# Kernel tuning notes

Hardware: AMD Instinct MI355X
Metric: run time of the kernel (lower is better)

## Reference

```python
import jax, jax.numpy as jnp
import numpy as np

BINS = 5
POINTS = 2
EPS_DIV = 1e-6
GN_GROUPS = 32
GN_EPS = 1e-5


def bilinear_sum(img, ys, xs):
    """Sum of bilinear samples with zero padding outside the image.
    img: (B, C, H, W); ys, xs: (B, K, H, W) absolute sample coords.
    Returns (B, C, H, W) = sum over K of bilinear(img, ys_k, xs_k)."""
    B, C, H, W = img.shape
    K = ys.shape[1]
    y0 = jnp.floor(ys)
    x0 = jnp.floor(xs)
    imgf = img.reshape(B, C, H * W)
    acc = jnp.zeros((B, C, K, H, W), img.dtype)
    for dy, dx in ((0, 0), (0, 1), (1, 0), (1, 1)):
        yi = y0 + dy
        xi = x0 + dx
        w = (1.0 - jnp.abs(ys - yi)) * (1.0 - jnp.abs(xs - xi))
        valid = (yi >= 0) & (yi <= H - 1) & (xi >= 0) & (xi <= W - 1)
        yc = jnp.clip(yi, 0, H - 1).astype(jnp.int32)
        xc = jnp.clip(xi, 0, W - 1).astype(jnp.int32)
        idx = (yc * W + xc).reshape(B, 1, K * H * W)
        g = jnp.take_along_axis(imgf, idx, axis=2).reshape(B, C, K, H, W)
        acc = acc + (w * valid.astype(img.dtype))[:, None] * g
    return acc.sum(axis=2)


def setup_inputs():
    key = jax.random.key(0)
    ks = jax.random.split(key, 6)
    B, C, H, W = 2, 256, 100, 152
    P, K = POINTS, BINS
    x = jax.random.normal(ks[0], (B, C, H, W), jnp.float32)
    offsets = jax.random.normal(ks[1], (B, P * K * 2, H, W), jnp.float32) * 2.0
    ef_w = jax.random.normal(ks[2], (P * C, C), jnp.float32) * 0.02
    ef_b = jnp.zeros((P * C,), jnp.float32)
    hm1_w = jax.random.normal(ks[3], (P, C, C), jnp.float32) * 0.02
    hm1_b = jnp.zeros((P, C), jnp.float32)
    hm2_w = jax.random.normal(ks[4], (P, C), jnp.float32) * 0.02
    hm2_b = jnp.zeros((P,), jnp.float32)
    merge_w = jax.random.normal(ks[5], (C, P * C), jnp.float32) * 0.02
    merge_b = jnp.zeros((C,), jnp.float32)
    gn_g = jnp.ones((C,), jnp.float32)
    gn_b = jnp.zeros((C,), jnp.float32)
    return {"x": x, "offsets": offsets, "ef_w": ef_w, "ef_b": ef_b,
            "hm1_w": hm1_w, "hm1_b": hm1_b, "hm2_w": hm2_w, "hm2_b": hm2_b,
            "merge_w": merge_w, "merge_b": merge_b, "gn_g": gn_g, "gn_b": gn_b}


def reference(x, offsets, ef_w, ef_b, hm1_w, hm1_b, hm2_w, hm2_b, merge_w, merge_b, gn_g, gn_b):
    B, C, H, W = x.shape
    P, K = POINTS, BINS
    # expand_feat: 1x1 conv C -> P*C
    ef = jnp.einsum('bchw,dc->bdhw', x, ef_w) + ef_b[None, :, None, None]
    efp = ef.reshape(B, P, C, H, W)
    # heatmap: grouped 1x1 conv (per-point) -> ReLU -> grouped 1x1 conv -> exp
    h = jax.nn.relu(jnp.einsum('bpchw,pdc->bpdhw', efp, hm1_w) + hm1_b[None, :, :, None, None])
    heat = jnp.exp(jnp.einsum('bpdhw,pd->bphw', h, hm2_w) + hm2_b[None, :, None, None])  # (B,P,H,W)
    # offsets: (B, P, K, 2, H, W) with channel layout [y, x] per bin.
    # base_offset cancels the [1,bins] kernel grid, so the deform conv with
    # all-ones weights is simply: sum over bins of bilinear samples at
    # (h + off_y, w + off_x).
    off = offsets.reshape(B, P, K, 2, H, W)
    hg = jnp.arange(H, dtype=x.dtype)[None, None, None, :, None]
    wg = jnp.arange(W, dtype=x.dtype)[None, None, None, None, :]
    ys = hg + off[:, :, :, 0]  # (B,P,K,H,W)
    xs = wg + off[:, :, :, 1]
    outs = []
    for p in range(P):
        # sample feat*heat (C channels) and heat (1 channel) together
        img = jnp.concatenate([efp[:, p] * heat[:, p][:, None], heat[:, p][:, None]], axis=1)
        s = bilinear_sum(img, ys[:, p], xs[:, p])  # (B, C+1, H, W)
        outs.append(s[:, :C] / (s[:, C:] + EPS_DIV))
    outs = jnp.concatenate(outs, axis=1)  # (B, P*C, H, W)
    merged = jnp.einsum('bchw,dc->bdhw', outs, merge_w) + merge_b[None, :, None, None]
    # GroupNorm(32, C) + ReLU
    g = merged.reshape(B, GN_GROUPS, C // GN_GROUPS, H, W)
    mu = g.mean(axis=(2, 3, 4), keepdims=True)
    var = g.var(axis=(2, 3, 4), keepdims=True)
    gn = ((g - mu) / jnp.sqrt(var + GN_EPS)).reshape(B, C, H, W)
    gn = gn * gn_g[None, :, None, None] + gn_b[None, :, None, None]
    return jax.nn.relu(gn)
```

## Files before the change

kernel.cpp:

```cpp
#include <hip/hip_runtime.h>

#define BINS 5
#define PTS  2
constexpr int Bx = 2, Cc = 256, Hh = 100, Ww = 152;
constexpr int HW = Hh * Ww;
constexpr int NTILE = 238;
constexpr float EPS_DIV = 1e-6f;
constexpr float GN_EPS  = 1e-5f;

typedef __attribute__((ext_vector_type(8)))  _Float16 hfrag;
typedef __attribute__((ext_vector_type(2)))  _Float16 h2;
typedef __attribute__((ext_vector_type(16))) float    f32x16;

__device__ __forceinline__ ushort f2h(float f) {
    return __builtin_bit_cast(ushort, (_Float16)f);
}
__device__ __forceinline__ float hlo(unsigned u) {
    return (float)__builtin_bit_cast(_Float16, (ushort)(u & 0xffffu));
}
__device__ __forceinline__ float hhi(unsigned u) {
    return (float)__builtin_bit_cast(_Float16, (ushort)(u >> 16));
}

#define GLL16(g, l) __builtin_amdgcn_global_load_lds( \
    (const __attribute__((address_space(1))) unsigned*)(g), \
    (__attribute__((address_space(3))) unsigned*)(l), 16, 0, 0)

#define MFMA32(a, b, c) __builtin_amdgcn_mfma_f32_32x32x16_f16(a, b, c, 0, 0, 0)

__global__ __launch_bounds__(256)
void k_wconv(const float* __restrict__ efw, const float* __restrict__ w1,
             const float* __restrict__ mw, ushort* __restrict__ wb)
{
    int gid = blockIdx.x * 256 + threadIdx.x;
    int i = gid * 8;
    int arr = i >> 17, off = i & 131071;
    const float* src = arr == 0 ? efw : (arr == 1 ? w1 : mw);
    float4 v0 = *(const float4*)(src + off);
    float4 v1 = *(const float4*)(src + off + 4);
    int outaddr;
    if (arr == 0) {
        int m = off >> 8, k = off & 255;
        outaddr = (((k >> 4) * 16 + (m >> 5)) * 64 + (m & 31) + 32 * ((k >> 3) & 1)) * 8;
    } else if (arr == 1) {
        int p = off >> 16, r = off & 65535;
        int m = r >> 8, k = r & 255;
        outaddr = p * 65536 +
                  (((k >> 4) * 8 + (m >> 5)) * 64 + (m & 31) + 32 * ((k >> 3) & 1)) * 8;
    } else {
        int m = off >> 9, k = off & 511;
        outaddr = (((k >> 4) * 8 + (m >> 5)) * 64 + (m & 31) + 32 * ((k >> 3) & 1)) * 8;
    }
    ushort o[8] = { f2h(v0.x), f2h(v0.y), f2h(v0.z), f2h(v0.w),
                    f2h(v1.x), f2h(v1.y), f2h(v1.z), f2h(v1.w) };
    *(uint4*)(wb + arr * 131072 + outaddr) = *(uint4*)o;
}

__global__ __launch_bounds__(256)
void k_xt(const float* __restrict__ x, ushort* __restrict__ xbt)
{
    __shared__ float tile[32][33];
    const int t = threadIdx.x;
    const int hw0 = blockIdx.x * 32;
    const int c0 = blockIdx.y * 32;
    const int b = blockIdx.z;
    const float* xb = x + ((size_t)b * Cc + c0) * HW + hw0;
    const int tx = t & 31, ty = t >> 5;
    #pragma unroll
    for (int r = 0; r < 4; r++) {
        int c = ty + r * 8;
        tile[c][tx] = xb[(size_t)c * HW + tx];
    }
    __syncthreads();
    const int hwl = t >> 3, c4 = (t & 7) * 4;
    ushort4 o = { f2h(tile[c4 + 0][hwl]), f2h(tile[c4 + 1][hwl]),
                  f2h(tile[c4 + 2][hwl]), f2h(tile[c4 + 3][hwl]) };
    *(ushort4*)&xbt[((size_t)b * HW + hw0 + hwl) * Cc + c0 + c4] = o;
}

__global__ __launch_bounds__(512, 2)
void k_ef(const ushort* __restrict__ xbt, const ushort* __restrict__ wbe,
          const float* __restrict__ efb, ushort* __restrict__ efp)
{
    __shared__ ushort B0[64 * 256];
    __shared__ ushort B1[64 * 256];
    const int t = threadIdx.x;
    const int wv = t >> 6, ln = t & 63;
    const int l31 = ln & 31, lh = ln >> 5;
    const int b = blockIdx.y;
    const int tt0 = blockIdx.x * 2;
    const ushort* xb = xbt + (size_t)b * HW * Cc;

    hfrag A[2][16];
    #pragma unroll
    for (int mf = 0; mf < 2; mf++)
        #pragma unroll
        for (int ks = 0; ks < 16; ks++)
            A[mf][ks] = *(const hfrag*)&wbe[((ks * 16 + (wv * 2 + mf)) * 64 + ln) * 8];
    __builtin_amdgcn_sched_barrier(0);

    auto stageB = [&](int tt, ushort* dst) {
        int tp0 = tt * 64;
        #pragma unroll
        for (int j = 0; j < 4; j++) {
            int unit = j * 512 + t;
            int prow = unit >> 5, c8 = unit & 31;
            int pq = tp0 + prow; if (pq > HW - 1) pq = HW - 1;
            const ushort* g = xb + (size_t)pq * Cc + ((c8 ^ (prow & 7)) << 3);
            ushort* l = dst + (j * 512 + wv * 64) * 8;
            GLL16(g, l);
        }
    };
    stageB(tt0, B0);
    stageB(tt0 + 1, B1);
    __builtin_amdgcn_sched_barrier(0);
    asm volatile("s_waitcnt vmcnt(4)" ::: "memory");
    __builtin_amdgcn_s_barrier();
    __builtin_amdgcn_sched_barrier(0);

    auto compute = [&](int tt, const ushort* Bs) {
        f32x16 acc[2][2];
        #pragma unroll
        for (int mf = 0; mf < 2; mf++)
            #pragma unroll
            for (int pf = 0; pf < 2; pf++)
                #pragma unroll
                for (int r = 0; r < 16; r++) acc[mf][pf][r] = 0.f;
        #pragma unroll
        for (int ks = 0; ks < 16; ks++) {
            int c = ks * 2 + lh;
            #pragma unroll
            for (int pf = 0; pf < 2; pf++) {
                hfrag bf = *(const hfrag*)&Bs[(pf * 32 + l31) * 256 + ((c ^ (l31 & 7)) << 3)];
                acc[0][pf] = MFMA32(A[0][ks], bf, acc[0][pf]);
                acc[1][pf] = MFMA32(A[1][ks], bf, acc[1][pf]);
            }
        }
        const int tp0 = tt * 64;
        const int p_ = wv >> 2;
        ushort* outb = efp + (size_t)((b * PTS + p_) * HW) * Cc;
        #pragma unroll
        for (int mf = 0; mf < 2; mf++) {
            int m0 = wv * 2 + mf;
            int chb = (m0 * 32) & 255;
            #pragma unroll
            for (int q = 0; q < 4; q++) {
                float4 bv = *(const float4*)&efb[m0 * 32 + q * 8 + 4 * lh];
                #pragma unroll
                for (int pf = 0; pf < 2; pf++) {
                    int px = tp0 + pf * 32 + l31;
                    if (px < HW) {
                        int ch = chb + q * 8 + 4 * lh;
                        ushort4 o = { f2h(acc[mf][pf][q * 4 + 0] + bv.x),
                                      f2h(acc[mf][pf][q * 4 + 1] + bv.y),
                                      f2h(acc[mf][pf][q * 4 + 2] + bv.z),
                                      f2h(acc[mf][pf][q * 4 + 3] + bv.w) };
                        *(ushort4*)&outb[(size_t)px * Cc + ch] = o;
                    }
                }
            }
        }
    };
    compute(tt0, B0);
    asm volatile("s_waitcnt vmcnt(0)" ::: "memory");
    __builtin_amdgcn_s_barrier();
    __builtin_amdgcn_sched_barrier(0);
    compute(tt0 + 1, B1);
}

__global__ __launch_bounds__(512, 2)
void k_heat(const ushort* __restrict__ efp, const ushort* __restrict__ wb1,
            const float* __restrict__ b1, const float* __restrict__ w2,
            const float* __restrict__ b2, float* __restrict__ heat)
{
    __shared__ ushort B0[64 * 256];
    __shared__ ushort B1[64 * 256];
    __shared__ float red[8][64];
    const int t = threadIdx.x;
    const int wv = t >> 6, ln = t & 63;
    const int l31 = ln & 31, lh = ln >> 5;
    const int zz = blockIdx.y;
    const int b = zz >> 1, p = zz & 1;
    const int tt0 = blockIdx.x * 2;
    const ushort* eb = efp + (size_t)((b * PTS + p) * HW) * Cc;
    const float* b1p = b1 + p * 256;
    const float* w2p = w2 + p * 256;
    const float b2v = b2[p];

    hfrag A[16];
    #pragma unroll
    for (int ks = 0; ks < 16; ks++)
        A[ks] = *(const hfrag*)&wb1[p * 65536 + ((ks * 8 + wv) * 64 + ln) * 8];
    __builtin_amdgcn_sched_barrier(0);

    auto stageB = [&](int tt, ushort* dst) {
        int tp0 = tt * 64;
        #pragma unroll
        for (int j = 0; j < 4; j++) {
            int unit = j * 512 + t;
            int prow = unit >> 5, c8 = unit & 31;
            int pq = tp0 + prow; if (pq > HW - 1) pq = HW - 1;
            const ushort* g = eb + (size_t)pq * Cc + ((c8 ^ (prow & 7)) << 3);
            ushort* l = dst + (j * 512 + wv * 64) * 8;
            GLL16(g, l);
        }
    };
    stageB(tt0, B0);
    stageB(tt0 + 1, B1);
    __builtin_amdgcn_sched_barrier(0);
    asm volatile("s_waitcnt vmcnt(4)" ::: "memory");
    __builtin_amdgcn_s_barrier();
    __builtin_amdgcn_sched_barrier(0);

    auto compute = [&](int tt, const ushort* Bs) {
        f32x16 acc[2];
        #pragma unroll
        for (int pf = 0; pf < 2; pf++)
            #pragma unroll
            for (int r = 0; r < 16; r++) acc[pf][r] = 0.f;
        #pragma unroll
        for (int ks = 0; ks < 16; ks++) {
            int c = ks * 2 + lh;
            #pragma unroll
            for (int pf = 0; pf < 2; pf++) {
                hfrag bf = *(const hfrag*)&Bs[(pf * 32 + l31) * 256 + ((c ^ (l31 & 7)) << 3)];
                acc[pf] = MFMA32(A[ks], bf, acc[pf]);
            }
        }
        float s[2] = {0.f, 0.f};
        #pragma unroll
        for (int q = 0; q < 4; q++) {
            float4 b1v = *(const float4*)&b1p[wv * 32 + q * 8 + 4 * lh];
            float4 w2v = *(const float4*)&w2p[wv * 32 + q * 8 + 4 * lh];
            #pragma unroll
            for (int pf = 0; pf < 2; pf++) {
                float h0 = acc[pf][q * 4 + 0] + b1v.x;
                float h1 = acc[pf][q * 4 + 1] + b1v.y;
                float h2_ = acc[pf][q * 4 + 2] + b1v.z;
                float h3 = acc[pf][q * 4 + 3] + b1v.w;
                s[pf] += w2v.x * (h0 > 0.f ? h0 : 0.f);
                s[pf] += w2v.y * (h1 > 0.f ? h1 : 0.f);
                s[pf] += w2v.z * (h2_ > 0.f ? h2_ : 0.f);
                s[pf] += w2v.w * (h3 > 0.f ? h3 : 0.f);
            }
        }
        s[0] += __shfl_xor(s[0], 32);
        s[1] += __shfl_xor(s[1], 32);
        if (lh == 0) {
            red[wv][l31]      = s[0];
            red[wv][32 + l31] = s[1];
        }
        asm volatile("s_waitcnt lgkmcnt(0)" ::: "memory");
        __builtin_amdgcn_s_barrier();
        if (t < 64) {
            float v = red[0][t] + red[1][t] + red[2][t] + red[3][t] +
                      red[4][t] + red[5][t] + red[6][t] + red[7][t];
            int px = tt * 64 + t;
            if (px < HW) heat[(size_t)(b * PTS + p) * HW + px] = expf(v + b2v);
        }
    };
    compute(tt0, B0);
    asm volatile("s_waitcnt vmcnt(0)" ::: "memory");
    __builtin_amdgcn_s_barrier();
    __builtin_amdgcn_sched_barrier(0);
    compute(tt0 + 1, B1);
}

__global__ __launch_bounds__(256)
void k_sample(const ushort* __restrict__ efp, const float* __restrict__ heat,
              const float* __restrict__ offs, ushort* __restrict__ outs)
{
    __shared__ uint2 s_wo[32][20];
    const int t = threadIdx.x;
    const int bid = blockIdx.x;
    const int nx = (bid & 7) * 60 + (bid >> 3);
    if (nx >= 475) return;
    const int m0 = nx * 32;
    const int p = blockIdx.y;
    const int b = blockIdx.z;
    const float* heat_bp = heat + (size_t)(b * PTS + p) * HW;

    if (t < 32 * BINS) {
        int j = t / BINS, k = t % BINS;
        int hw = m0 + j;
        int hh = hw / Ww, ww = hw % Ww;
        int chy = (p * BINS + k) * 2;
        float oy = offs[((size_t)b * (PTS * BINS * 2) + chy)     * HW + hw];
        float ox = offs[((size_t)b * (PTS * BINS * 2) + chy + 1) * HW + hw];
        float ysf = (float)hh + oy;
        float xsf = (float)ww + ox;
        float y0 = floorf(ysf), x0 = floorf(xsf);
        #pragma unroll
        for (int dy = 0; dy < 2; dy++)
            #pragma unroll
            for (int dx = 0; dx < 2; dx++) {
                float yi = y0 + dy, xi = x0 + dx;
                float wgt = (1.f - fabsf(ysf - yi)) * (1.f - fabsf(xsf - xi));
                bool valid = (yi >= 0.f) && (yi <= (float)(Hh - 1)) &&
                             (xi >= 0.f) && (xi <= (float)(Ww - 1));
                int yc = (int)yi; yc = yc < 0 ? 0 : (yc > Hh - 1 ? Hh - 1 : yc);
                int xc = (int)xi; xc = xc < 0 ? 0 : (xc > Ww - 1 ? Ww - 1 : xc);
                int idx = yc * Ww + xc;
                float wh = valid ? wgt * heat_bp[idx] : 0.f;
                s_wo[j][k * 4 + dy * 2 + dx] =
                    make_uint2(__float_as_uint(wh), (unsigned)idx << 9);
            }
    }
    __syncthreads();
    if (t < 32) {
        float s = 0.f;
        #pragma unroll
        for (int u = 0; u < 20; u++) s += __uint_as_float(s_wo[t][u].x);
        float inv = 1.f / (s + EPS_DIV);
        #pragma unroll
        for (int u = 0; u < 20; u++) {
            float w = __uint_as_float(s_wo[t][u].x) * inv;
            unsigned hw16 = (unsigned)f2h(w);
            s_wo[t][u].x = hw16 | (hw16 << 16);
        }
    }
    __syncthreads();

    const int wv = t >> 6, ln = t & 63;
    const int half = ln >> 5, c8 = ln & 31;
    const char* efbase = (const char*)(efp + (size_t)((b * PTS + p) * HW) * Cc)
                         + c8 * 16;
    ushort* ob = outs + ((size_t)(b * HW + m0)) * (PTS * Cc) + p * Cc + c8 * 8;
    #pragma unroll
    for (int i = 0; i < 8; i += 2) {
        const int j = wv * 8 + i + half;
        h2 a0 = (h2){0, 0}, a1 = (h2){0, 0}, a2 = (h2){0, 0}, a3 = (h2){0, 0};
        #pragma unroll
        for (int u = 0; u < 20; u++) {
            uint2 wo = s_wo[j][u];
            uint4 v = *(const uint4*)(efbase + wo.y);
            h2 wp = __builtin_bit_cast(h2, wo.x);
            a0 += wp * __builtin_bit_cast(h2, v.x);
            a1 += wp * __builtin_bit_cast(h2, v.y);
            a2 += wp * __builtin_bit_cast(h2, v.z);
            a3 += wp * __builtin_bit_cast(h2, v.w);
        }
        uint4 o = { __builtin_bit_cast(unsigned, a0), __builtin_bit_cast(unsigned, a1),
                    __builtin_bit_cast(unsigned, a2), __builtin_bit_cast(unsigned, a3) };
        *(uint4*)(ob + (size_t)j * (PTS * Cc)) = o;
    }
}

__global__ __launch_bounds__(512, 2)
void k_merge(const ushort* __restrict__ outs, const ushort* __restrict__ wbm,
             const float* __restrict__ mb, ushort* __restrict__ mgb,
             float* __restrict__ part2)
{
    __shared__ ushort B0[64 * 512];
    __shared__ ushort B1[64 * 512];
    const int t = threadIdx.x;
    const int wv = t >> 6, ln = t & 63;
    const int l31 = ln & 31, lh = ln >> 5;
    const int b = blockIdx.y;
    const int tt0 = blockIdx.x * 2;
    const ushort* ob = outs + (size_t)b * HW * (PTS * Cc);

    hfrag A[32];
    #pragma unroll
    for (int ks = 0; ks < 32; ks++)
        A[ks] = *(const hfrag*)&wbm[((ks * 8 + wv) * 64 + ln) * 8];
    __builtin_amdgcn_sched_barrier(0);

    auto stageB = [&](int tt, ushort* dst) {
        int tp0 = tt * 64;
        #pragma unroll
        for (int j = 0; j < 8; j++) {
            int unit = j * 512 + t;
            int prow = unit >> 6, c8 = unit & 63;
            int pq = tp0 + prow; if (pq > HW - 1) pq = HW - 1;
            const ushort* g = ob + (size_t)pq * (PTS * Cc) + ((c8 ^ (prow & 7)) << 3);
            ushort* l = dst + (j * 512 + wv * 64) * 8;
            GLL16(g, l);
        }
    };
    stageB(tt0, B0);
    stageB(tt0 + 1, B1);
    __builtin_amdgcn_sched_barrier(0);
    asm volatile("s_waitcnt vmcnt(8)" ::: "memory");
    __builtin_amdgcn_s_barrier();
    __builtin_amdgcn_sched_barrier(0);

    auto compute = [&](int tt, const ushort* Bs) {
        f32x16 acc[2];
        #pragma unroll
        for (int pf = 0; pf < 2; pf++)
            #pragma unroll
            for (int r = 0; r < 16; r++) acc[pf][r] = 0.f;
        #pragma unroll
        for (int ks = 0; ks < 32; ks++) {
            int c = ks * 2 + lh;
            #pragma unroll
            for (int pf = 0; pf < 2; pf++) {
                hfrag bf = *(const hfrag*)&Bs[(pf * 32 + l31) * 512 + ((c ^ (l31 & 7)) << 3)];
                acc[pf] = MFMA32(A[ks], bf, acc[pf]);
            }
        }
        const int tp0 = tt * 64;
        float sg[4] = {0.f, 0.f, 0.f, 0.f};
        float qg[4] = {0.f, 0.f, 0.f, 0.f};
        #pragma unroll
        for (int q = 0; q < 4; q++) {
            float4 bv = *(const float4*)&mb[wv * 32 + q * 8 + 4 * lh];
            #pragma unroll
            for (int pf = 0; pf < 2; pf++) {
                int px = tp0 + pf * 32 + l31;
                if (px < HW) {
                    #pragma unroll
                    for (int r = 0; r < 4; r++) {
                        float bb = r == 0 ? bv.x : (r == 1 ? bv.y : (r == 2 ? bv.z : bv.w));
                        float v = acc[pf][q * 4 + r] + bb;
                        int ch = wv * 32 + q * 8 + 4 * lh + r;
                        mgb[((size_t)b * Cc + ch) * HW + px] = f2h(v);
                        sg[q] += v; qg[q] += v * v;
                    }
                }
            }
        }
        #pragma unroll
        for (int q = 0; q < 4; q++) {
            #pragma unroll
            for (int off = 1; off <= 32; off <<= 1) {
                sg[q] += __shfl_xor(sg[q], off);
                qg[q] += __shfl_xor(qg[q], off);
            }
        }
        if (ln == 0) {
            #pragma unroll
            for (int q = 0; q < 4; q++) {
                int g = wv * 4 + q;
                size_t idx = ((size_t)(b * 32 + g) * NTILE + tt) * 2;
                part2[idx + 0] = sg[q];
                part2[idx + 1] = qg[q];
            }
        }
    };
    compute(tt0, B0);
    asm volatile("s_waitcnt vmcnt(0)" ::: "memory");
    __builtin_amdgcn_s_barrier();
    __builtin_amdgcn_sched_barrier(0);
    compute(tt0 + 1, B1);
}

__global__ __launch_bounds__(256)
void k_gnfinal(const float* __restrict__ part2, float* __restrict__ statf)
{
    const int bg = blockIdx.x;
    const int t = threadIdx.x;
    float s = 0.f, q = 0.f;
    if (t < NTILE) {
        s = part2[((size_t)bg * NTILE + t) * 2 + 0];
        q = part2[((size_t)bg * NTILE + t) * 2 + 1];
    }
    #pragma unroll
    for (int off = 1; off <= 32; off <<= 1) {
        s += __shfl_xor(s, off);
        q += __shfl_xor(q, off);
    }
    __shared__ float rs[4], rq[4];
    int wid = t >> 6;
    if ((t & 63) == 0) { rs[wid] = s; rq[wid] = q; }
    __syncthreads();
    if (t == 0) {
        float S = rs[0] + rs[1] + rs[2] + rs[3];
        float Q = rq[0] + rq[1] + rq[2] + rq[3];
        const float n = 8.f * HW;
        float mean = S / n;
        float var  = Q / n - mean * mean;
        statf[bg * 2 + 0] = mean;
        statf[bg * 2 + 1] = rsqrtf(var + GN_EPS);
    }
}

__global__ __launch_bounds__(256)
void k_gnapply(const ushort* __restrict__ mgb, const float* __restrict__ statf,
               const float* __restrict__ gg, const float* __restrict__ gb,
               float* __restrict__ out)
{
    const int i8 = blockIdx.x * 256 + threadIdx.x;
    const int i = i8 * 8;
    const int CHW = Cc * HW;
    const int b = i / CHW;
    const int r = i - b * CHW;
    const int c = r / HW;
    const int g = c >> 3;
    float mean = statf[(b * 32 + g) * 2 + 0];
    float istd = statf[(b * 32 + g) * 2 + 1];
    float sc = istd * gg[c];
    float sh = gb[c] - mean * sc;
    uint4 v = *(const uint4*)(mgb + i);
    float4 o0, o1;
    o0.x = fmaxf(hlo(v.x) * sc + sh, 0.f);
    o0.y = fmaxf(hhi(v.x) * sc + sh, 0.f);
    o0.z = fmaxf(hlo(v.y) * sc + sh, 0.f);
    o0.w = fmaxf(hhi(v.y) * sc + sh, 0.f);
    o1.x = fmaxf(hlo(v.z) * sc + sh, 0.f);
    o1.y = fmaxf(hhi(v.z) * sc + sh, 0.f);
    o1.z = fmaxf(hlo(v.w) * sc + sh, 0.f);
    o1.w = fmaxf(hhi(v.w) * sc + sh, 0.f);
    *(float4*)(out + i)     = o0;
    *(float4*)(out + i + 4) = o1;
}

extern "C" void kernel_launch(void* const* d_in, const int* in_sizes, int n_in,
                              void* d_out, int out_size, void* d_ws, size_t ws_size,
                              hipStream_t stream)
{
    const float* x    = (const float*)d_in[0];
    const float* offs = (const float*)d_in[1];
    const float* efw  = (const float*)d_in[2];
    const float* efb  = (const float*)d_in[3];
    const float* w1   = (const float*)d_in[4];
    const float* b1   = (const float*)d_in[5];
    const float* w2   = (const float*)d_in[6];
    const float* b2   = (const float*)d_in[7];
    const float* mw   = (const float*)d_in[8];
    const float* mb   = (const float*)d_in[9];
    const float* gg   = (const float*)d_in[10];
    const float* gb   = (const float*)d_in[11];
    float* out = (float*)d_out;

    ushort* wb    = (ushort*)d_ws;
    ushort* wbe   = wb;
    ushort* wb1   = wb + 131072;
    ushort* wbm   = wb + 262144;
    ushort* efp   = wb + 393216;
    ushort* outsb = efp + (size_t)Bx * PTS * HW * Cc;
    ushort* xbt   = outsb + (size_t)Bx * HW * PTS * Cc;
    ushort* mgb   = xbt + (size_t)Bx * HW * Cc;
    float*  heat  = (float*)(mgb + (size_t)Bx * Cc * HW);
    float*  part2 = heat + (size_t)Bx * PTS * HW;
    float*  statf = part2 + (size_t)64 * NTILE * 2;

    dim3 blk(256);
    k_wconv  <<<dim3(192),              blk, 0, stream>>>(efw, w1, mw, wb);
    k_xt     <<<dim3(475, 8, Bx),       blk, 0, stream>>>(x, xbt);
    k_ef     <<<dim3(119, Bx),    dim3(512), 0, stream>>>(xbt, wbe, efb, efp);
    k_heat   <<<dim3(119, 4),     dim3(512), 0, stream>>>(efp, wb1, b1, w2, b2, heat);
    k_sample <<<dim3(480, PTS, Bx),     blk, 0, stream>>>(efp, heat, offs, outsb);
    k_merge  <<<dim3(119, Bx),    dim3(512), 0, stream>>>(outsb, wbm, mb, mgb, part2);
    k_gnfinal<<<dim3(64),               blk, 0, stream>>>(part2, statf);
    k_gnapply<<<dim3(Bx * Cc * HW / 8 / 256), blk, 0, stream>>>(mgb, statf, gg, gb, out);
}
```

Baseline: 206.3 us.

## Fuse bilinear sampling into merge GEMM and merge weight/input prep kernels

The sampling stage now writes its per-tile results straight into a swizzled LDS buffer, and the merge MFMA GEMM reads its B operand from there, so the intermediate sampled-feature tensor no longer round-trips through global memory. Merge weights are loaded in chunks of eight fragments to cut register pressure. The weight conversion and input transpose kernels are combined into one launch. The fused kernel loses the previous double-buffered async global-to-LDS prefetch and serialises sampling, barriers and GEMM inside each block, which may leave fewer blocks in flight. The ef output-point index is also now derived per fragment (m0>>3) rather than per wave.

```diff
diff --git a/kernel.cpp b/kernel.cpp
--- a/kernel.cpp
+++ b/kernel.cpp
@@ -29,53 +29,54 @@
 #define MFMA32(a, b, c) __builtin_amdgcn_mfma_f32_32x32x16_f16(a, b, c, 0, 0, 0)
 
 __global__ __launch_bounds__(256)
-void k_wconv(const float* __restrict__ efw, const float* __restrict__ w1,
-             const float* __restrict__ mw, ushort* __restrict__ wb)
-{
-    int gid = blockIdx.x * 256 + threadIdx.x;
-    int i = gid * 8;
-    int arr = i >> 17, off = i & 131071;
-    const float* src = arr == 0 ? efw : (arr == 1 ? w1 : mw);
-    float4 v0 = *(const float4*)(src + off);
-    float4 v1 = *(const float4*)(src + off + 4);
-    int outaddr;
-    if (arr == 0) {
-        int m = off >> 8, k = off & 255;
-        outaddr = (((k >> 4) * 16 + (m >> 5)) * 64 + (m & 31) + 32 * ((k >> 3) & 1)) * 8;
-    } else if (arr == 1) {
-        int p = off >> 16, r = off & 65535;
-        int m = r >> 8, k = r & 255;
-        outaddr = p * 65536 +
-                  (((k >> 4) * 8 + (m >> 5)) * 64 + (m & 31) + 32 * ((k >> 3) & 1)) * 8;
+void k_pre(const float* __restrict__ efw, const float* __restrict__ w1,
+           const float* __restrict__ mw, ushort* __restrict__ wb,
+           const float* __restrict__ x, ushort* __restrict__ xbt)
+{
+    __shared__ float tile[32][33];
+    const int bid = blockIdx.x;
+    const int t = threadIdx.x;
+    if (bid < 192) {
+        int gid = bid * 256 + t;
+        int i = gid * 8;
+        int arr = i >> 17, off = i & 131071;
+        const float* src = arr == 0 ? efw : (arr == 1 ? w1 : mw);
+        float4 v0 = *(const float4*)(src + off);
+        float4 v1 = *(const float4*)(src + off + 4);
+        int outaddr;
+        if (arr == 0) {
+            int m = off >> 8, k = off & 255;
+            outaddr = (((k >> 4) * 16 + (m >> 5)) * 64 + (m & 31) + 32 * ((k >> 3) & 1)) * 8;
+        } else if (arr == 1) {
+            int p = off >> 16, r = off & 65535;
+            int m = r >> 8, k = r & 255;
+            outaddr = p * 65536 +
+                      (((k >> 4) * 8 + (m >> 5)) * 64 + (m & 31) + 32 * ((k >> 3) & 1)) * 8;
+        } else {
+            int m = off >> 9, k = off & 511;
+            outaddr = (((k >> 4) * 8 + (m >> 5)) * 64 + (m & 31) + 32 * ((k >> 3) & 1)) * 8;
+        }
+        ushort o[8] = { f2h(v0.x), f2h(v0.y), f2h(v0.z), f2h(v0.w),
+                        f2h(v1.x), f2h(v1.y), f2h(v1.z), f2h(v1.w) };
+        *(uint4*)(wb + arr * 131072 + outaddr) = *(uint4*)o;
     } else {
-        int m = off >> 9, k = off & 511;
-        outaddr = (((k >> 4) * 8 + (m >> 5)) * 64 + (m & 31) + 32 * ((k >> 3) & 1)) * 8;
-    }
-    ushort o[8] = { f2h(v0.x), f2h(v0.y), f2h(v0.z), f2h(v0.w),
-                    f2h(v1.x), f2h(v1.y), f2h(v1.z), f2h(v1.w) };
-    *(uint4*)(wb + arr * 131072 + outaddr) = *(uint4*)o;
-}
-
-__global__ __launch_bounds__(256)
-void k_xt(const float* __restrict__ x, ushort* __restrict__ xbt)
-{
-    __shared__ float tile[32][33];
-    const int t = threadIdx.x;
-    const int hw0 = blockIdx.x * 32;
-    const int c0 = blockIdx.y * 32;
-    const int b = blockIdx.z;
-    const float* xb = x + ((size_t)b * Cc + c0) * HW + hw0;
-    const int tx = t & 31, ty = t >> 5;
-    #pragma unroll
-    for (int r = 0; r < 4; r++) {
-        int c = ty + r * 8;
-        tile[c][tx] = xb[(size_t)c * HW + tx];
-    }
-    __syncthreads();
-    const int hwl = t >> 3, c4 = (t & 7) * 4;
-    ushort4 o = { f2h(tile[c4 + 0][hwl]), f2h(tile[c4 + 1][hwl]),
-                  f2h(tile[c4 + 2][hwl]), f2h(tile[c4 + 3][hwl]) };
-    *(ushort4*)&xbt[((size_t)b * HW + hw0 + hwl) * Cc + c0 + c4] = o;
+        int r = bid - 192;
+        const int b = r / 3800; r -= b * 3800;
+        const int c0 = (r / 475) * 32;
+        const int hw0 = (r % 475) * 32;
+        const float* xb = x + ((size_t)b * Cc + c0) * HW + hw0;
+        const int tx = t & 31, ty = t >> 5;
+        #pragma unroll
+        for (int rr = 0; rr < 4; rr++) {
+            int c = ty + rr * 8;
+            tile[c][tx] = xb[(size_t)c * HW + tx];
+        }
+        __syncthreads();
+        const int hwl = t >> 3, c4 = (t & 7) * 4;
+        ushort4 o = { f2h(tile[c4 + 0][hwl]), f2h(tile[c4 + 1][hwl]),
+                      f2h(tile[c4 + 2][hwl]), f2h(tile[c4 + 3][hwl]) };
+        *(ushort4*)&xbt[((size_t)b * HW + hw0 + hwl) * Cc + c0 + c4] = o;
+    }
 }
 
 __global__ __launch_bounds__(512, 2)
@@ -137,11 +138,11 @@
             }
         }
         const int tp0 = tt * 64;
-        const int p_ = wv >> 2;
-        ushort* outb = efp + (size_t)((b * PTS + p_) * HW) * Cc;
         #pragma unroll
         for (int mf = 0; mf < 2; mf++) {
             int m0 = wv * 2 + mf;
+            const int p_ = m0 >> 3;
+            ushort* outb = efp + (size_t)((b * PTS + p_) * HW) * Cc;
             int chb = (m0 * 32) & 255;
             #pragma unroll
             for (int q = 0; q < 4; q++) {
@@ -266,184 +267,158 @@
     compute(tt0 + 1, B1);
 }
 
-__global__ __launch_bounds__(256)
-void k_sample(const ushort* __restrict__ efp, const float* __restrict__ heat,
-              const float* __restrict__ offs, ushort* __restrict__ outs)
-{
-    __shared__ uint2 s_wo[32][20];
-    const int t = threadIdx.x;
-    const int bid = blockIdx.x;
-    const int nx = (bid & 7) * 60 + (bid >> 3);
-    if (nx >= 475) return;
-    const int m0 = nx * 32;
-    const int p = blockIdx.y;
-    const int b = blockIdx.z;
-    const float* heat_bp = heat + (size_t)(b * PTS + p) * HW;
-
-    if (t < 32 * BINS) {
-        int j = t / BINS, k = t % BINS;
-        int hw = m0 + j;
-        int hh = hw / Ww, ww = hw % Ww;
-        int chy = (p * BINS + k) * 2;
-        float oy = offs[((size_t)b * (PTS * BINS * 2) + chy)     * HW + hw];
-        float ox = offs[((size_t)b * (PTS * BINS * 2) + chy + 1) * HW + hw];
-        float ysf = (float)hh + oy;
-        float xsf = (float)ww + ox;
-        float y0 = floorf(ysf), x0 = floorf(xsf);
-        #pragma unroll
-        for (int dy = 0; dy < 2; dy++)
-            #pragma unroll
-            for (int dx = 0; dx < 2; dx++) {
-                float yi = y0 + dy, xi = x0 + dx;
-                float wgt = (1.f - fabsf(ysf - yi)) * (1.f - fabsf(xsf - xi));
-                bool valid = (yi >= 0.f) && (yi <= (float)(Hh - 1)) &&
-                             (xi >= 0.f) && (xi <= (float)(Ww - 1));
-                int yc = (int)yi; yc = yc < 0 ? 0 : (yc > Hh - 1 ? Hh - 1 : yc);
-                int xc = (int)xi; xc = xc < 0 ? 0 : (xc > Ww - 1 ? Ww - 1 : xc);
-                int idx = yc * Ww + xc;
-                float wh = valid ? wgt * heat_bp[idx] : 0.f;
-                s_wo[j][k * 4 + dy * 2 + dx] =
-                    make_uint2(__float_as_uint(wh), (unsigned)idx << 9);
-            }
-    }
-    __syncthreads();
-    if (t < 32) {
-        float s = 0.f;
-        #pragma unroll
-        for (int u = 0; u < 20; u++) s += __uint_as_float(s_wo[t][u].x);
-        float inv = 1.f / (s + EPS_DIV);
-        #pragma unroll
-        for (int u = 0; u < 20; u++) {
-            float w = __uint_as_float(s_wo[t][u].x) * inv;
-            unsigned hw16 = (unsigned)f2h(w);
-            s_wo[t][u].x = hw16 | (hw16 << 16);
-        }
-    }
-    __syncthreads();
-
-    const int wv = t >> 6, ln = t & 63;
-    const int half = ln >> 5, c8 = ln & 31;
-    const char* efbase = (const char*)(efp + (size_t)((b * PTS + p) * HW) * Cc)
-                         + c8 * 16;
-    ushort* ob = outs + ((size_t)(b * HW + m0)) * (PTS * Cc) + p * Cc + c8 * 8;
-    #pragma unroll
-    for (int i = 0; i < 8; i += 2) {
-        const int j = wv * 8 + i + half;
-        h2 a0 = (h2){0, 0}, a1 = (h2){0, 0}, a2 = (h2){0, 0}, a3 = (h2){0, 0};
-        #pragma unroll
-        for (int u = 0; u < 20; u++) {
-            uint2 wo = s_wo[j][u];
-            uint4 v = *(const uint4*)(efbase + wo.y);
-            h2 wp = __builtin_bit_cast(h2, wo.x);
-            a0 += wp * __builtin_bit_cast(h2, v.x);
-            a1 += wp * __builtin_bit_cast(h2, v.y);
-            a2 += wp * __builtin_bit_cast(h2, v.z);
-            a3 += wp * __builtin_bit_cast(h2, v.w);
-        }
-        uint4 o = { __builtin_bit_cast(unsigned, a0), __builtin_bit_cast(unsigned, a1),
-                    __builtin_bit_cast(unsigned, a2), __builtin_bit_cast(unsigned, a3) };
-        *(uint4*)(ob + (size_t)j * (PTS * Cc)) = o;
-    }
-}
-
 __global__ __launch_bounds__(512, 2)
-void k_merge(const ushort* __restrict__ outs, const ushort* __restrict__ wbm,
-             const float* __restrict__ mb, ushort* __restrict__ mgb,
-             float* __restrict__ part2)
-{
-    __shared__ ushort B0[64 * 512];
-    __shared__ ushort B1[64 * 512];
+void k_sm(const ushort* __restrict__ efp, const float* __restrict__ heat,
+          const float* __restrict__ offs, const ushort* __restrict__ wbm,
+          const float* __restrict__ mb, ushort* __restrict__ mgb,
+          float* __restrict__ part2)
+{
+    __shared__ ushort Bs[64 * 512];
+    __shared__ uint2 s_wo[64][20];
     const int t = threadIdx.x;
     const int wv = t >> 6, ln = t & 63;
     const int l31 = ln & 31, lh = ln >> 5;
+    const int bid = blockIdx.x;
+    const int tile = (bid & 7) * 30 + (bid >> 3);
+    if (tile >= NTILE) return;
     const int b = blockIdx.y;
-    const int tt0 = blockIdx.x * 2;
-    const ushort* ob = outs + (size_t)b * HW * (PTS * Cc);
-
-    hfrag A[32];
+    const int m0 = tile * 64;
+
+    for (int p = 0; p < PTS; p++) {
+        const float* heat_bp = heat + (size_t)(b * PTS + p) * HW;
+        if (t < 64 * BINS) {
+            int j = t / BINS, k = t - (t / BINS) * BINS;
+            int hw = m0 + j;
+            bool ok = hw < HW;
+            int hwc = ok ? hw : HW - 1;
+            int hh = hwc / Ww, ww = hwc - hh * Ww;
+            int chy = (p * BINS + k) * 2;
+            float oy = offs[((size_t)b * (PTS * BINS * 2) + chy)     * HW + hwc];
+            float ox = offs[((size_t)b * (PTS * BINS * 2) + chy + 1) * HW + hwc];
+            float ysf = (float)hh + oy;
+            float xsf = (float)ww + ox;
+            float y0 = floorf(ysf), x0 = floorf(xsf);
+            #pragma unroll
+            for (int dy = 0; dy < 2; dy++)
+                #pragma unroll
+                for (int dx = 0; dx < 2; dx++) {
+                    float yi = y0 + dy, xi = x0 + dx;
+                    float wgt = (1.f - fabsf(ysf - yi)) * (1.f - fabsf(xsf - xi));
+                    bool valid = ok && (yi >= 0.f) && (yi <= (float)(Hh - 1)) &&
+                                 (xi >= 0.f) && (xi <= (float)(Ww - 1));
+                    int yc = (int)yi; yc = yc < 0 ? 0 : (yc > Hh - 1 ? Hh - 1 : yc);
+                    int xc = (int)xi; xc = xc < 0 ? 0 : (xc > Ww - 1 ? Ww - 1 : xc);
+                    int idx = yc * Ww + xc;
+                    float wh = valid ? wgt * heat_bp[idx] : 0.f;
+                    s_wo[j][k * 4 + dy * 2 + dx] =
+                        make_uint2(__float_as_uint(wh), (unsigned)idx << 9);
+                }
+        }
+        asm volatile("s_waitcnt lgkmcnt(0)" ::: "memory");
+        __builtin_amdgcn_s_barrier();
+        __builtin_amdgcn_sched_barrier(0);
+        if (t < 64) {
+            float s = 0.f;
+            #pragma unroll
+            for (int u = 0; u < 20; u++) s += __uint_as_float(s_wo[t][u].x);
+            float inv = 1.f / (s + EPS_DIV);
+            #pragma unroll
+            for (int u = 0; u < 20; u++) {
+                float w = __uint_as_float(s_wo[t][u].x) * inv;
+                unsigned hw16 = (unsigned)f2h(w);
+                s_wo[t][u].x = hw16 | (hw16 << 16);
+            }
+        }
+        asm volatile("s_waitcnt lgkmcnt(0)" ::: "memory");
+        __builtin_amdgcn_s_barrier();
+        __builtin_amdgcn_sched_barrier(0);
+
+        const int half = lh, c8 = l31;
+        const char* efbase = (const char*)(efp + (size_t)((b * PTS + p) * HW) * Cc)
+                             + c8 * 16;
+        const int g = p * 32 + c8;
+        #pragma unroll
+        for (int i = 0; i < 8; i += 2) {
+            const int j = wv * 8 + i + half;
+            h2 a0 = (h2){0, 0}, a1 = (h2){0, 0}, a2 = (h2){0, 0}, a3 = (h2){0, 0};
+            #pragma unroll
+            for (int u = 0; u < 20; u++) {
+                uint2 wo = s_wo[j][u];
+                uint4 v = *(const uint4*)(efbase + wo.y);
+                h2 wp = __builtin_bit_cast(h2, wo.x);
+                a0 += wp * __builtin_bit_cast(h2, v.x);
+                a1 += wp * __builtin_bit_cast(h2, v.y);
+                a2 += wp * __builtin_bit_cast(h2, v.z);
+                a3 += wp * __builtin_bit_cast(h2, v.w);
+            }
+            uint4 o = { __builtin_bit_cast(unsigned, a0), __builtin_bit_cast(unsigned, a1),
+                        __builtin_bit_cast(unsigned, a2), __builtin_bit_cast(unsigned, a3) };
+            *(uint4*)&Bs[j * 512 + ((g ^ (j & 7)) << 3)] = o;
+        }
+        asm volatile("s_waitcnt lgkmcnt(0)" ::: "memory");
+        __builtin_amdgcn_s_barrier();
+        __builtin_amdgcn_sched_barrier(0);
+    }
+
+    f32x16 acc[2];
     #pragma unroll
-    for (int ks = 0; ks < 32; ks++)
-        A[ks] = *(const hfrag*)&wbm[((ks * 8 + wv) * 64 + ln) * 8];
-    __builtin_amdgcn_sched_barrier(0);
-
-    auto stageB = [&](int tt, ushort* dst) {
-        int tp0 = tt * 64;
-        #pragma unroll
-        for (int j = 0; j < 8; j++) {
-            int unit = j * 512 + t;
-            int prow = unit >> 6, c8 = unit & 63;
-            int pq = tp0 + prow; if (pq > HW - 1) pq = HW - 1;
-            const ushort* g = ob + (size_t)pq * (PTS * Cc) + ((c8 ^ (prow & 7)) << 3);
-            ushort* l = dst + (j * 512 + wv * 64) * 8;
-            GLL16(g, l);
-        }
-    };
-    stageB(tt0, B0);
-    stageB(tt0 + 1, B1);
-    __builtin_amdgcn_sched_barrier(0);
-    asm volatile("s_waitcnt vmcnt(8)" ::: "memory");
-    __builtin_amdgcn_s_barrier();
-    __builtin_amdgcn_sched_barrier(0);
-
-    auto compute = [&](int tt, const ushort* Bs) {
-        f32x16 acc[2];
-        #pragma unroll
-        for (int pf = 0; pf < 2; pf++)
-            #pragma unroll
-            for (int r = 0; r < 16; r++) acc[pf][r] = 0.f;
-        #pragma unroll
-        for (int ks = 0; ks < 32; ks++) {
-            int c = ks * 2 + lh;
+    for (int pf = 0; pf < 2; pf++)
+        #pragma unroll
+        for (int r = 0; r < 16; r++) acc[pf][r] = 0.f;
+    #pragma unroll 1
+    for (int c4 = 0; c4 < 4; c4++) {
+        hfrag A8[8];
+        #pragma unroll
+        for (int k8 = 0; k8 < 8; k8++)
+            A8[k8] = *(const hfrag*)&wbm[(((c4 * 8 + k8) * 8 + wv) * 64 + ln) * 8];
+        #pragma unroll
+        for (int k8 = 0; k8 < 8; k8++) {
+            int c = (c4 * 8 + k8) * 2 + lh;
             #pragma unroll
             for (int pf = 0; pf < 2; pf++) {
                 hfrag bf = *(const hfrag*)&Bs[(pf * 32 + l31) * 512 + ((c ^ (l31 & 7)) << 3)];
-                acc[pf] = MFMA32(A[ks], bf, acc[pf]);
-            }
-        }
-        const int tp0 = tt * 64;
-        float sg[4] = {0.f, 0.f, 0.f, 0.f};
-        float qg[4] = {0.f, 0.f, 0.f, 0.f};
+                acc[pf] = MFMA32(A8[k8], bf, acc[pf]);
+            }
+        }
+    }
+
+    float sg[4] = {0.f, 0.f, 0.f, 0.f};
+    float qg[4] = {0.f, 0.f, 0.f, 0.f};
+    #pragma unroll
+    for (int q = 0; q < 4; q++) {
+        float4 bv = *(const float4*)&mb[wv * 32 + q * 8 + 4 * lh];
+        #pragma unroll
+        for (int pf = 0; pf < 2; pf++) {
+            int px = m0 + pf * 32 + l31;
+            if (px < HW) {
+                #pragma unroll
+                for (int r = 0; r < 4; r++) {
+                    float bb = r == 0 ? bv.x : (r == 1 ? bv.y : (r == 2 ? bv.z : bv.w));
+                    float v = acc[pf][q * 4 + r] + bb;
+                    int ch = wv * 32 + q * 8 + 4 * lh + r;
+                    mgb[((size_t)b * Cc + ch) * HW + px] = f2h(v);
+                    sg[q] += v; qg[q] += v * v;
+                }
+            }
+        }
+    }
+    #pragma unroll
+    for (int q = 0; q < 4; q++) {
+        #pragma unroll
+        for (int off = 1; off <= 32; off <<= 1) {
+            sg[q] += __shfl_xor(sg[q], off);
+            qg[q] += __shfl_xor(qg[q], off);
+        }
+    }
+    if (ln == 0) {
         #pragma unroll
         for (int q = 0; q < 4; q++) {
-            float4 bv = *(const float4*)&mb[wv * 32 + q * 8 + 4 * lh];
-            #pragma unroll
-            for (int pf = 0; pf < 2; pf++) {
-                int px = tp0 + pf * 32 + l31;
-                if (px < HW) {
-                    #pragma unroll
-                    for (int r = 0; r < 4; r++) {
-                        float bb = r == 0 ? bv.x : (r == 1 ? bv.y : (r == 2 ? bv.z : bv.w));
-                        float v = acc[pf][q * 4 + r] + bb;
-                        int ch = wv * 32 + q * 8 + 4 * lh + r;
-                        mgb[((size_t)b * Cc + ch) * HW + px] = f2h(v);
-                        sg[q] += v; qg[q] += v * v;
-                    }
-                }
-            }
-        }
-        #pragma unroll
-        for (int q = 0; q < 4; q++) {
-            #pragma unroll
-            for (int off = 1; off <= 32; off <<= 1) {
-                sg[q] += __shfl_xor(sg[q], off);
-                qg[q] += __shfl_xor(qg[q], off);
-            }
-        }
-        if (ln == 0) {
-            #pragma unroll
-            for (int q = 0; q < 4; q++) {
-                int g = wv * 4 + q;
-                size_t idx = ((size_t)(b * 32 + g) * NTILE + tt) * 2;
-                part2[idx + 0] = sg[q];
-                part2[idx + 1] = qg[q];
-            }
-        }
-    };
-    compute(tt0, B0);
-    asm volatile("s_waitcnt vmcnt(0)" ::: "memory");
-    __builtin_amdgcn_s_barrier();
-    __builtin_amdgcn_sched_barrier(0);
-    compute(tt0 + 1, B1);
+            int g = wv * 4 + q;
+            size_t idx = ((size_t)(b * 32 + g) * NTILE + tile) * 2;
+            part2[idx + 0] = sg[q];
+            part2[idx + 1] = qg[q];
+        }
+    }
 }
 
 __global__ __launch_bounds__(256)
@@ -537,12 +512,10 @@
     float*  statf = part2 + (size_t)64 * NTILE * 2;
 
     dim3 blk(256);
-    k_wconv  <<<dim3(192),              blk, 0, stream>>>(efw, w1, mw, wb);
-    k_xt     <<<dim3(475, 8, Bx),       blk, 0, stream>>>(x, xbt);
+    k_pre    <<<dim3(7792),             blk, 0, stream>>>(efw, w1, mw, wb, x, xbt);
     k_ef     <<<dim3(119, Bx),    dim3(512), 0, stream>>>(xbt, wbe, efb, efp);
     k_heat   <<<dim3(119, 4),     dim3(512), 0, stream>>>(efp, wb1, b1, w2, b2, heat);
-    k_sample <<<dim3(480, PTS, Bx),     blk, 0, stream>>>(efp, heat, offs, outsb);
-    k_merge  <<<dim3(119, Bx),    dim3(512), 0, stream>>>(outsb, wbm, mb, mgb, part2);
+    k_sm     <<<dim3(240, Bx),    dim3(512), 0, stream>>>(efp, heat, offs, wbm, mb, mgb, part2);
     k_gnfinal<<<dim3(64),               blk, 0, stream>>>(part2, statf);
     k_gnapply<<<dim3(Bx * Cc * HW / 8 / 256), blk, 0, stream>>>(mgb, statf, gg, gb, out);
 }
```

Result: faster. 198.2 us (-3.9%).
